# Performance work log

Hardware: AMD Instinct MI355X
Metric: run time of the kernel (lower is better)

Reference implementation:

```python
import jax, jax.numpy as jnp
import numpy as np

N = 16000        # nodes
E = 256000       # edges
D_IN = 1280      # input node features
HID = 256        # hidden dim (all hidden_dims equal; required by res_linear shapes)
HEADS = 8
C = HID // HEADS # 32 channels per head
G = 32           # graphs in the batch
O = 64           # output labels (GO terms)
NB = 2           # conv blocks = len(hidden_dims) - 1
EPS = 1e-5


def _bn(h, g, b):
    # eval-mode BatchNorm1d with running_mean=0, running_var=1 (init state)
    return h * (g / jnp.sqrt(1.0 + EPS)) + b


def _seg_softmax(logits, seg, num):
    # numerically-stable segment softmax (PyG softmax semantics)
    m = jax.ops.segment_max(logits, seg, num_segments=num)
    e = jnp.exp(logits - m[seg])
    s = jax.ops.segment_sum(e, seg, num_segments=num)
    return e / (s[seg] + 1e-16)


def setup_inputs() -> dict:
    key = jax.random.key(0)
    ks = jax.random.split(key, 16)
    w = lambda i, sh: jax.random.normal(ks[i], sh, jnp.float32) * 0.05
    return {
        "x": jax.random.normal(ks[0], (N, D_IN), jnp.float32),
        "edge_index": jax.random.randint(ks[1], (2, E), 0, N),
        "batch": jnp.sort(jax.random.randint(ks[2], (N,), 0, G)),
        # feature_proj: Linear -> ReLU -> BN
        "fp_W": w(3, (D_IN, HID)), "fp_b": jnp.zeros(HID),
        "fp_g": jnp.ones(HID), "fp_be": jnp.zeros(HID),
        # GATv2Conv per block: lin_l, lin_r, att, out-bias
        "gat_Wl": w(4, (NB, HID, HID)), "gat_bl": jnp.zeros((NB, HID)),
        "gat_Wr": w(5, (NB, HID, HID)), "gat_br": jnp.zeros((NB, HID)),
        "gat_att": w(6, (NB, HEADS, C)), "gat_bias": jnp.zeros((NB, HID)),
        # GINConv MLP: Linear -> ReLU -> BN
        "gin_W": w(7, (NB, HID, HID)), "gin_b": jnp.zeros((NB, HID)),
        "gin_g": jnp.ones((NB, HID)), "gin_be": jnp.zeros((NB, HID)),
        # PyG LayerNorm (graph mode) affine
        "ln_g": jnp.ones((NB, HID)), "ln_b": jnp.zeros((NB, HID)),
        # residual linears
        "res_W": w(8, (NB, HID, HID)), "res_b": jnp.zeros((NB, HID)),
        # GlobalAttention gate MLP
        "pool_W1": w(9, (HID, HID)), "pool_b1": jnp.zeros(HID),
        "pool_W2": w(10, (HID, 1)), "pool_b2": jnp.zeros(1),
        # O label heads (hierarchy=None -> just the MLP), stacked
        "head_W1": w(11, (O, HID, 256)), "head_b1": jnp.zeros((O, 256)),
        "head_g": jnp.ones((O, 256)), "head_be": jnp.zeros((O, 256)),
        "head_W2": w(12, (O, 256)), "head_b2": jnp.zeros(O),
    }


def reference(x, edge_index, batch, fp_W, fp_b, fp_g, fp_be,
              gat_Wl, gat_bl, gat_Wr, gat_br, gat_att, gat_bias,
              gin_W, gin_b, gin_g, gin_be, ln_g, ln_b, res_W, res_b,
              pool_W1, pool_b1, pool_W2, pool_b2,
              head_W1, head_b1, head_g, head_be, head_W2, head_b2):
    n = x.shape[0]
    # feature_proj (eval: dropout = identity)
    h = _bn(jax.nn.relu(x @ fp_W + fp_b), fp_g, fp_be)

    src0, dst0 = edge_index[0], edge_index[1]
    loop = jnp.arange(n)
    src = jnp.concatenate([src0, loop])  # GATv2 adds self-loops by default
    dst = jnp.concatenate([dst0, loop])

    for i in range(NB):
        # ---- GATv2Conv (no activation after, per original control flow) ----
        xl = (h @ gat_Wl[i] + gat_bl[i]).reshape(n, HEADS, C)
        xr = (h @ gat_Wr[i] + gat_br[i]).reshape(n, HEADS, C)
        msg = xl[src]                                   # [E', H, C]
        eact = jax.nn.leaky_relu(msg + xr[dst], 0.2)
        logit = jnp.einsum('ehc,hc->eh', eact, gat_att[i])
        alpha = _seg_softmax(logit, dst, n)             # [E', H]
        h = jax.ops.segment_sum(alpha[:, :, None] * msg, dst,
                                num_segments=n).reshape(n, HID) + gat_bias[i]
        # ---- GINConv: nn((1+0)*x + sum_neighbors), then leaky_relu ----
        agg = jax.ops.segment_sum(h[src0], dst0, num_segments=n)
        gin = _bn(jax.nn.relu((h + agg) @ gin_W[i] + gin_b[i]), gin_g[i], gin_be[i])
        h = jax.nn.leaky_relu(gin, 0.2)
        # ---- PyG LayerNorm (graph mode, batch=None: global mean/std) + residual ----
        mu = h.mean()
        sd = jnp.std(h)
        ln = (h - mu) / (sd + EPS) * ln_g[i] + ln_b[i]
        h = jax.nn.leaky_relu(ln + (h @ res_W[i] + res_b[i]), 0.2)

    # ---- GlobalAttention pooling ----
    gate = jnp.tanh(h @ pool_W1 + pool_b1) @ pool_W2 + pool_b2   # [N, 1]
    a = _seg_softmax(gate[:, 0], batch, G)
    emb = jax.ops.segment_sum(a[:, None] * h, batch, num_segments=G)  # [G, HID]

    # ---- O label heads (hierarchy None -> MLP only), vectorized ----
    z = jnp.einsum('bd,odh->boh', emb, head_W1) + head_b1[None]
    z = _bn(jax.nn.silu(z), head_g[None], head_be[None])
    out = jnp.einsum('boh,oh->bo', z, head_W2) + head_b2[None]
    return out[:, :, None]  # torch.stack(outputs, dim=1) -> [G, O, 1]
```

## Files before the change

kernel.cpp:

```cpp
#include <hip/hip_runtime.h>
#include <math.h>

#define N_NODES 16000
#define N_EDGES 256000
#define EPE (N_EDGES + N_NODES)
#define DIN 1280
#define HID 256
#define HEADS 8
#define CPH 32
#define NG 32
#define NO 64
#define EPSC 1e-5f
#define SPAD 40

typedef __bf16 bf16;
typedef __attribute__((ext_vector_type(8))) __bf16 bf16x8;
typedef __attribute__((ext_vector_type(4))) float floatx4;

__device__ __forceinline__ float lrelu(float v) { return v > 0.f ? v : 0.2f * v; }
__device__ __forceinline__ float bflo(unsigned int u) { return __uint_as_float(u << 16); }
__device__ __forceinline__ float bfhi(unsigned int u) { return __uint_as_float(u & 0xffff0000u); }
__device__ __forceinline__ unsigned int bfpack(float x, float y) {
    bf16 b0 = (bf16)x, b1 = (bf16)y;
    return ((unsigned int)*(unsigned short*)&b0) | (((unsigned int)*(unsigned short*)&b1) << 16);
}

__global__ void wconv_gen(const float* __restrict__ W, bf16* __restrict__ Wt, int K, int total) {
    int idx = blockIdx.x * 256 + threadIdx.x;
    if (idx >= total) return;
    int per = K * HID;
    int l = idx / per, rem = idx - l * per;
    int n = rem / K, k = rem - n * K;
    Wt[idx] = (bf16)W[(size_t)l * per + (size_t)k * HID + n];
}

__global__ void wconv_pair(const float* __restrict__ Wl, const float* __restrict__ Wr,
                           bf16* __restrict__ Wt) {
    int idx = blockIdx.x * 256 + threadIdx.x;
    int n = idx >> 8, k = idx & 255;
    float v = (n < 256) ? Wl[(size_t)k * HID + n] : Wr[(size_t)k * HID + (n - 256)];
    Wt[idx] = (bf16)v;
}

__global__ __launch_bounds__(256) void gemm64(
    const bf16* __restrict__ A, const bf16* __restrict__ Bt,
    const float* __restrict__ bias, const float* __restrict__ bias2,
    bf16* __restrict__ C, int K, int ldc, int mode,
    const float* __restrict__ g, const float* __restrict__ be,
    float2* __restrict__ statp, const float* __restrict__ stat)
{
    __shared__ __align__(16) bf16 As[2][64 * SPAD];
    __shared__ __align__(16) bf16 Bs[2][64 * SPAD];
    const int tid = threadIdx.x;
    const int bm = blockIdx.y * 64, bn = blockIdx.x * 64;
    const int w = tid >> 6, lane = tid & 63;
    const int wm = w * 16;
    const int lrow = lane & 15, lk8 = (lane >> 4) * 8;
    const int row = tid >> 2, k8 = (tid & 3) * 8;

    const bf16* gA = A + (size_t)(bm + row) * K + k8;
    const bf16* gB = Bt + (size_t)(bn + row) * K + k8;

    floatx4 acc[4];
#pragma unroll
    for (int j = 0; j < 4; j++) acc[j] = (floatx4){0.f, 0.f, 0.f, 0.f};

    const int nk = K >> 5;
    bf16x8 ra = *(const bf16x8*)gA;
    bf16x8 rb = *(const bf16x8*)gB;

    for (int it = 0; it < nk; ++it) {
        int p = it & 1;
        *(bf16x8*)&As[p][row * SPAD + k8] = ra;
        *(bf16x8*)&Bs[p][row * SPAD + k8] = rb;
        __syncthreads();
        if (it + 1 < nk) {
            ra = *(const bf16x8*)(gA + (it + 1) * 32);
            rb = *(const bf16x8*)(gB + (it + 1) * 32);
        }
        bf16x8 af = *(const bf16x8*)&As[p][(wm + lrow) * SPAD + lk8];
        bf16x8 bfr[4];
#pragma unroll
        for (int j = 0; j < 4; j++) bfr[j] = *(const bf16x8*)&Bs[p][(16 * j + lrow) * SPAD + lk8];
#pragma unroll
        for (int j = 0; j < 4; j++)
            acc[j] = __builtin_amdgcn_mfma_f32_16x16x32_bf16(af, bfr[j], acc[j], 0, 0, 0);
    }

    const float inv = rsqrtf(1.f + EPSC);
    const int row0 = bm + wm + (lane >> 4) * 4;
    float mu = 0.f, rs = 0.f;
    if (mode == 3) {
        const float inv_n = 1.f / (float)((size_t)N_NODES * HID);
        mu = stat[0] * inv_n;
        float var = stat[1] * inv_n - mu * mu;
        rs = 1.f / (sqrtf(fmaxf(var, 0.f)) + EPSC);
    }
    float sz = 0.f, sq = 0.f;
#pragma unroll
    for (int j = 0; j < 4; j++) {
        int col = bn + 16 * j + lrow;
        float bcol = (col < HID) ? bias[col] : bias2[col - HID];
        float gc = (mode >= 2) ? g[col] : 0.f;
        float bec = (mode >= 2) ? be[col] : 0.f;
#pragma unroll
        for (int r = 0; r < 4; r++) {
            float z = acc[j][r] + bcol;
            if (mode == 2) {
                z = fmaxf(z, 0.f) * (gc * inv) + bec;
                z = lrelu(z);
                sz += z; sq += z * z;
            } else if (mode == 3) {
                float h = (float)A[(size_t)(row0 + r) * K + col];
                z = (h - mu) * rs * gc + bec + z;
                z = lrelu(z);
            }
            C[(size_t)(row0 + r) * ldc + col] = (bf16)z;
        }
    }
    if (mode == 2) {
        for (int o = 32; o > 0; o >>= 1) { sz += __shfl_down(sz, o); sq += __shfl_down(sq, o); }
        __syncthreads();
        float* rs_ = (float*)&As[0][0];
        float* rq_ = (float*)&Bs[0][0];
        if (lane == 0) { rs_[w] = sz; rq_[w] = sq; }
        __syncthreads();
        if (tid == 0)
            statp[blockIdx.y * gridDim.x + blockIdx.x] =
                make_float2(rs_[0] + rs_[1] + rs_[2] + rs_[3],
                            rq_[0] + rq_[1] + rq_[2] + rq_[3]);
    }
}

__global__ __launch_bounds__(256, 1) void gemm_f32A(
    const float* __restrict__ A, const bf16* __restrict__ Bt,
    const float* __restrict__ bias, bf16* __restrict__ C, int K,
    const float* __restrict__ g, const float* __restrict__ be)
{
    __shared__ __align__(16) bf16 As[2][128 * SPAD];
    __shared__ __align__(16) bf16 Bs[2][128 * SPAD];
    const int tid = threadIdx.x;
    const int bm = blockIdx.y * 128, bn = blockIdx.x * 128;
    const int w = tid >> 6, lane = tid & 63;
    const int wm = (w & 1) * 64, wn = (w >> 1) * 64;
    const int lrow = lane & 15, lk8 = (lane >> 4) * 8;

    floatx4 acc[4][4];
#pragma unroll
    for (int i = 0; i < 4; i++)
#pragma unroll
        for (int j = 0; j < 4; j++) acc[i][j] = (floatx4){0.f, 0.f, 0.f, 0.f};

    const int r2 = tid >> 1, c2 = tid & 1;
    const float* gA = A + (size_t)(bm + r2) * K + c2 * 16;
    const bf16* gB = Bt + (size_t)(bn + r2) * K + c2 * 16;
    bf16* sA = &As[0][r2 * SPAD + c2 * 16];
    bf16* sB = &Bs[0][r2 * SPAD + c2 * 16];

    const int nk = K >> 5;
    float4 a[4][4];
    bf16x8 b[4][2];
#pragma unroll
    for (int u = 0; u < 4; u++) {
        const float* pa = gA + u * 32;
        a[u][0] = *(const float4*)(pa + 0);
        a[u][1] = *(const float4*)(pa + 4);
        a[u][2] = *(const float4*)(pa + 8);
        a[u][3] = *(const float4*)(pa + 12);
        const bf16* pb = gB + u * 32;
        b[u][0] = *(const bf16x8*)(pb + 0);
        b[u][1] = *(const bf16x8*)(pb + 8);
    }

    for (int it0 = 0; it0 < nk; it0 += 4) {
#pragma unroll
        for (int u = 0; u < 4; u++) {
            const int it = it0 + u;
            const int p = u & 1;
            const int po = p * 128 * SPAD;
            bf16x8 h0, h1;
            h0[0] = (bf16)a[u][0].x; h0[1] = (bf16)a[u][0].y; h0[2] = (bf16)a[u][0].z; h0[3] = (bf16)a[u][0].w;
            h0[4] = (bf16)a[u][1].x; h0[5] = (bf16)a[u][1].y; h0[6] = (bf16)a[u][1].z; h0[7] = (bf16)a[u][1].w;
            h1[0] = (bf16)a[u][2].x; h1[1] = (bf16)a[u][2].y; h1[2] = (bf16)a[u][2].z; h1[3] = (bf16)a[u][2].w;
            h1[4] = (bf16)a[u][3].x; h1[5] = (bf16)a[u][3].y; h1[6] = (bf16)a[u][3].z; h1[7] = (bf16)a[u][3].w;
            *(bf16x8*)(sA + po + 0) = h0;
            *(bf16x8*)(sA + po + 8) = h1;
            *(bf16x8*)(sB + po + 0) = b[u][0];
            *(bf16x8*)(sB + po + 8) = b[u][1];
            __syncthreads();
            if (it + 4 < nk) {
                const float* pa = gA + (it + 4) * 32;
                a[u][0] = *(const float4*)(pa + 0);
                a[u][1] = *(const float4*)(pa + 4);
                a[u][2] = *(const float4*)(pa + 8);
                a[u][3] = *(const float4*)(pa + 12);
                const bf16* pb = gB + (it + 4) * 32;
                b[u][0] = *(const bf16x8*)(pb + 0);
                b[u][1] = *(const bf16x8*)(pb + 8);
            }
            bf16x8 af[4], bfr[4];
#pragma unroll
            for (int i = 0; i < 4; i++) af[i] = *(const bf16x8*)&As[p][(wm + 16 * i + lrow) * SPAD + lk8];
#pragma unroll
            for (int j = 0; j < 4; j++) bfr[j] = *(const bf16x8*)&Bs[p][(wn + 16 * j + lrow) * SPAD + lk8];
#pragma unroll
            for (int i = 0; i < 4; i++)
#pragma unroll
                for (int j = 0; j < 4; j++)
                    acc[i][j] = __builtin_amdgcn_mfma_f32_16x16x32_bf16(af[i], bfr[j], acc[i][j], 0, 0, 0);
        }
    }

    const float inv = rsqrtf(1.f + EPSC);
#pragma unroll
    for (int j = 0; j < 4; j++) {
        int col = bn + wn + 16 * j + lrow;
        float bcol = bias[col];
        float gc = g[col] * inv;
        float bec = be[col];
#pragma unroll
        for (int i = 0; i < 4; i++) {
            int row0 = bm + wm + 16 * i + (lane >> 4) * 4;
#pragma unroll
            for (int r = 0; r < 4; r++) {
                float z = fmaxf(acc[i][j][r] + bcol, 0.f) * gc + bec;
                C[(size_t)(row0 + r) * HID + col] = (bf16)z;
            }
        }
    }
}

__global__ void hist_kernel(const int* __restrict__ ei, int* __restrict__ cnt) {
    int e = blockIdx.x * 256 + threadIdx.x;
    if (e >= EPE) return;
    int d = (e < N_EDGES) ? ei[N_EDGES + e] : (e - N_EDGES);
    atomicAdd(&cnt[d], 1);
}

__global__ __launch_bounds__(1024) void scan_kernel(const int* __restrict__ cnt,
                                                    int* __restrict__ roff, int* __restrict__ cursor,
                                                    const int* __restrict__ batch,
                                                    int* __restrict__ gstart) {
    __shared__ int wsum[16];
    int t = threadIdx.x;
    int base = t * 16;
    int local[16]; int s = 0;
#pragma unroll
    for (int i = 0; i < 16; i++) {
        int idx = base + i;
        int v = (idx < N_NODES) ? cnt[idx] : 0;
        local[i] = s; s += v;
    }
    int lane = t & 63, wid = t >> 6;
    int incl = s;
    for (int o = 1; o < 64; o <<= 1) { int v = __shfl_up(incl, o); if (lane >= o) incl += v; }
    if (lane == 63) wsum[wid] = incl;
    __syncthreads();
    if (t == 0) { int a = 0; for (int k = 0; k < 16; k++) { int v = wsum[k]; wsum[k] = a; a += v; } }
    __syncthreads();
    int texcl = incl - s + wsum[wid];
#pragma unroll
    for (int i = 0; i < 16; i++) {
        int idx = base + i;
        if (idx < N_NODES) { int o = texcl + local[i]; roff[idx] = o; cursor[idx] = o; }
    }
    if (t == 1023) roff[N_NODES] = texcl + s;
    if (t <= NG) {
        int lo = 0, hi = N_NODES;
        while (lo < hi) { int mid = (lo + hi) >> 1; if (batch[mid] < t) lo = mid + 1; else hi = mid; }
        gstart[t] = lo;
    }
}

__global__ void scatter_kernel(const int* __restrict__ ei, int* __restrict__ cursor,
                               int* __restrict__ esrc) {
    int e = blockIdx.x * 256 + threadIdx.x;
    if (e >= EPE) return;
    int s, d;
    if (e < N_EDGES) { s = ei[e]; d = ei[N_EDGES + e]; }
    else { s = d = e - N_EDGES; }
    int pos = atomicAdd(&cursor[d], 1);
    esrc[pos] = s;
}

__global__ __launch_bounds__(256) void gat_wave(
    const bf16* __restrict__ XLR, const int* __restrict__ roff, const int* __restrict__ esrc,
    const float* __restrict__ att, const float* __restrict__ gbias, bf16* __restrict__ out)
{
    const int wid = threadIdx.x >> 6;
    const int lane = threadIdx.x & 63;
    const int d = blockIdx.x * 4 + wid;
    const int beg = roff[d], end = roff[d + 1];
    const int c0 = lane * 4;

    const unsigned int* xru = (const unsigned int*)(XLR + (size_t)d * 512 + 256 + c0);
    const unsigned int xr01 = xru[0], xr23 = xru[1];
    const float xr0 = bflo(xr01), xr1 = bfhi(xr01), xr2 = bflo(xr23), xr3 = bfhi(xr23);
    const float at0 = att[c0], at1 = att[c0 + 1], at2 = att[c0 + 2], at3 = att[c0 + 3];

    float m = -INFINITY, s = 0.f;
    float a0 = 0.f, a1 = 0.f, a2 = 0.f, a3 = 0.f;

    int src = esrc[beg];
    const unsigned int* xp = (const unsigned int*)(XLR + (size_t)src * 512 + c0);
    unsigned int xl01 = xp[0], xl23 = xp[1];

    for (int e = beg; e < end; ++e) {
        unsigned int nx01 = 0u, nx23 = 0u;
        if (e + 1 < end) {
            int ns = esrc[e + 1];
            const unsigned int* np = (const unsigned int*)(XLR + (size_t)ns * 512 + c0);
            nx01 = np[0]; nx23 = np[1];
        }
        float x0 = bflo(xl01), x1 = bfhi(xl01), x2 = bflo(xl23), x3 = bfhi(xl23);
        float p = lrelu(x0 + xr0) * at0 + lrelu(x1 + xr1) * at1
                + lrelu(x2 + xr2) * at2 + lrelu(x3 + xr3) * at3;
        p += __shfl_xor(p, 1);
        p += __shfl_xor(p, 2);
        p += __shfl_xor(p, 4);
        float mn = fmaxf(m, p);
        float rsc = __expf(m - mn);
        float wgt = __expf(p - mn);
        s = s * rsc + wgt;
        a0 = a0 * rsc + wgt * x0;
        a1 = a1 * rsc + wgt * x1;
        a2 = a2 * rsc + wgt * x2;
        a3 = a3 * rsc + wgt * x3;
        m = mn;
        xl01 = nx01; xl23 = nx23;
    }

    const float rinv = 1.f / (s + 1e-16f);
    float v0 = gbias[c0]     + a0 * rinv;
    float v1 = gbias[c0 + 1] + a1 * rinv;
    float v2 = gbias[c0 + 2] + a2 * rinv;
    float v3 = gbias[c0 + 3] + a3 * rinv;
    unsigned int* op = (unsigned int*)(out + (size_t)d * HID + c0);
    op[0] = bfpack(v0, v1);
    op[1] = bfpack(v2, v3);
}

__global__ __launch_bounds__(256) void gin_wave(
    const bf16* __restrict__ H, const int* __restrict__ roff,
    const int* __restrict__ esrc, bf16* __restrict__ U)
{
    const int wid = threadIdx.x >> 6;
    const int lane = threadIdx.x & 63;
    const int d = blockIdx.x * 4 + wid;
    const int beg = roff[d], end = roff[d + 1];
    const int c0 = lane * 4;

    float a0 = 0.f, a1 = 0.f, a2 = 0.f, a3 = 0.f;
    int e = beg;
    for (; e + 1 < end; e += 2) {
        int s0 = esrc[e], s1 = esrc[e + 1];
        const unsigned int* p0 = (const unsigned int*)(H + (size_t)s0 * HID + c0);
        const unsigned int* p1 = (const unsigned int*)(H + (size_t)s1 * HID + c0);
        unsigned int u01 = p0[0], u23 = p0[1];
        unsigned int v01 = p1[0], v23 = p1[1];
        a0 += bflo(u01) + bflo(v01);
        a1 += bfhi(u01) + bfhi(v01);
        a2 += bflo(u23) + bflo(v23);
        a3 += bfhi(u23) + bfhi(v23);
    }
    if (e < end) {
        const unsigned int* p0 = (const unsigned int*)(H + (size_t)esrc[e] * HID + c0);
        unsigned int u01 = p0[0], u23 = p0[1];
        a0 += bflo(u01); a1 += bfhi(u01); a2 += bflo(u23); a3 += bfhi(u23);
    }
    unsigned int* up = (unsigned int*)(U + (size_t)d * HID + c0);
    up[0] = bfpack(a0, a1);
    up[1] = bfpack(a2, a3);
}

__global__ void stats_reduce(const float2* __restrict__ part, float* __restrict__ stat, int n) {
    int t = threadIdx.x;
    float s = 0.f, q = 0.f;
    for (int i = t; i < n; i += 256) { float2 v = part[i]; s += v.x; q += v.y; }
    for (int o = 32; o > 0; o >>= 1) { s += __shfl_down(s, o); q += __shfl_down(q, o); }
    __shared__ float ls[4], lq[4];
    int wid = t >> 6, lane = t & 63;
    if (lane == 0) { ls[wid] = s; lq[wid] = q; }
    __syncthreads();
    if (t == 0) { stat[0] = ls[0] + ls[1] + ls[2] + ls[3]; stat[1] = lq[0] + lq[1] + lq[2] + lq[3]; }
}

__global__ __launch_bounds__(256) void pool_gate_kernel(const bf16* __restrict__ t,
    const float* __restrict__ W2, const float* __restrict__ b2, float* __restrict__ gate)
{
    int n = blockIdx.x * 4 + (threadIdx.x >> 6);
    int lane = threadIdx.x & 63;
    const bf16* p = t + (size_t)n * HID + lane * 4;
    float4 w = *(const float4*)(W2 + lane * 4);
    float s = tanhf((float)p[0]) * w.x + tanhf((float)p[1]) * w.y
            + tanhf((float)p[2]) * w.z + tanhf((float)p[3]) * w.w;
    for (int o = 32; o > 0; o >>= 1) s += __shfl_down(s, o);
    if (lane == 0) gate[n] = s + b2[0];
}

__global__ __launch_bounds__(256) void pool_stats_kernel(
    float* __restrict__ gate, const int* __restrict__ gstart)
{
    int g = blockIdx.x, t = threadIdx.x;
    int lo = gstart[g], hi = gstart[g + 1];
    __shared__ float red[256];
    float m = -INFINITY;
    for (int n = lo + t; n < hi; n += 256) m = fmaxf(m, gate[n]);
    red[t] = m; __syncthreads();
    for (int st = 128; st > 0; st >>= 1) { if (t < st) red[t] = fmaxf(red[t], red[t + st]); __syncthreads(); }
    m = red[0]; __syncthreads();
    float s = 0.f;
    for (int n = lo + t; n < hi; n += 256) s += __expf(gate[n] - m);
    red[t] = s; __syncthreads();
    for (int st = 128; st > 0; st >>= 1) { if (t < st) red[t] += red[t + st]; __syncthreads(); }
    float sinv = 1.f / (red[0] + 1e-16f);
    for (int n = lo + t; n < hi; n += 256) gate[n] = __expf(gate[n] - m) * sinv;
}

__global__ __launch_bounds__(256) void emb_accum_kernel(
    const float* __restrict__ a, const int* __restrict__ batch,
    const bf16* __restrict__ h, float* __restrict__ emb)
{
    int n0 = blockIdx.x * 32, t = threadIdx.x;
    int cur = batch[n0]; float acc = 0.f;
    for (int j = 0; j < 32; j++) {
        int n = n0 + j;
        int b = batch[n];
        if (b != cur) { atomicAdd(&emb[cur * HID + t], acc); cur = b; acc = 0.f; }
        acc += a[n] * (float)h[(size_t)n * HID + t];
    }
    atomicAdd(&emb[cur * HID + t], acc);
}

__global__ __launch_bounds__(256) void heads_kernel(
    const float* __restrict__ emb, const float* __restrict__ W1, const float* __restrict__ b1,
    const float* __restrict__ hg, const float* __restrict__ hbe, const float* __restrict__ W2,
    const float* __restrict__ b2, float* __restrict__ out)
{
    int o = blockIdx.x;
    int g0 = blockIdx.y * 4;
    int k = threadIdx.x;
    __shared__ float se[4][HID];
    __shared__ float red[256];
#pragma unroll
    for (int j = 0; j < 4; j++) se[j][k] = emb[(g0 + j) * HID + k];
    __syncthreads();
    const float* w1p = W1 + (size_t)o * HID * HID + k;
    float zb = b1[o * HID + k];
    float z0 = zb, z1 = zb, z2 = zb, z3 = zb;
#pragma unroll 8
    for (int d = 0; d < HID; d++) {
        float w = w1p[(size_t)d * HID];
        z0 = fmaf(se[0][d], w, z0);
        z1 = fmaf(se[1][d], w, z1);
        z2 = fmaf(se[2][d], w, z2);
        z3 = fmaf(se[3][d], w, z3);
    }
    const float gk = hg[o * HID + k] * rsqrtf(1.f + EPSC);
    const float bek = hbe[o * HID + k];
    const float w2 = W2[o * HID + k];
    const float b2o = b2[o];
    float zz[4] = {z0, z1, z2, z3};
#pragma unroll
    for (int j = 0; j < 4; j++) {
        float z = zz[j];
        float sil = z / (1.f + expf(-z));
        red[k] = (sil * gk + bek) * w2;
        __syncthreads();
        for (int st = 128; st > 0; st >>= 1) { if (k < st) red[k] += red[k + st]; __syncthreads(); }
        if (k == 0) out[(g0 + j) * NO + o] = red[0] + b2o;
        __syncthreads();
    }
}

extern "C" void kernel_launch(void* const* d_in, const int* in_sizes, int n_in,
                              void* d_out, int out_size, void* d_ws, size_t ws_size,
                              hipStream_t stream) {
    const float* x        = (const float*)d_in[0];
    const int*   ei       = (const int*)  d_in[1];
    const int*   batch    = (const int*)  d_in[2];
    const float* fp_W     = (const float*)d_in[3];
    const float* fp_b     = (const float*)d_in[4];
    const float* fp_g     = (const float*)d_in[5];
    const float* fp_be    = (const float*)d_in[6];
    const float* gat_Wl   = (const float*)d_in[7];
    const float* gat_bl   = (const float*)d_in[8];
    const float* gat_Wr   = (const float*)d_in[9];
    const float* gat_br   = (const float*)d_in[10];
    const float* gat_att  = (const float*)d_in[11];
    const float* gat_bias = (const float*)d_in[12];
    const float* gin_W    = (const float*)d_in[13];
    const float* gin_b    = (const float*)d_in[14];
    const float* gin_g    = (const float*)d_in[15];
    const float* gin_be   = (const float*)d_in[16];
    const float* ln_g     = (const float*)d_in[17];
    const float* ln_b     = (const float*)d_in[18];
    const float* res_W    = (const float*)d_in[19];
    const float* res_b    = (const float*)d_in[20];
    const float* pool_W1  = (const float*)d_in[21];
    const float* pool_b1  = (const float*)d_in[22];
    const float* pool_W2  = (const float*)d_in[23];
    const float* pool_b2  = (const float*)d_in[24];
    const float* head_W1  = (const float*)d_in[25];
    const float* head_b1  = (const float*)d_in[26];
    const float* head_g   = (const float*)d_in[27];
    const float* head_be  = (const float*)d_in[28];
    const float* head_W2  = (const float*)d_in[29];
    const float* head_b2  = (const float*)d_in[30];
    float* out = (float*)d_out;

    char* base = (char*)d_ws;
    size_t off = 0;
    auto alloc = [&](size_t bytes) -> char* {
        char* p = base + off; off += (bytes + 255) & ~(size_t)255; return p;
    };
    int*   esrc   = (int*)  alloc((size_t)EPE * 4);
    int*   cnt    = (int*)  alloc((size_t)N_NODES * 4);
    int*   roff   = (int*)  alloc((size_t)(N_NODES + 1) * 4);
    int*   cursor = (int*)  alloc((size_t)N_NODES * 4);
    float* gate   = (float*)alloc((size_t)N_NODES * 4);
    int*   gstart = (int*)  alloc((NG + 1) * 4);
    float* emb    = (float*)alloc(NG * HID * 4);
    float* stat   = (float*)alloc(8);
    float2* statp = (float2*)alloc(1024 * 8);
    bf16*  Hb0    = (bf16*) alloc((size_t)N_NODES * HID * 2);
    bf16*  Hb1    = (bf16*) alloc((size_t)N_NODES * HID * 2);
    bf16*  XLR    = (bf16*) alloc((size_t)N_NODES * 512 * 2);
    bf16*  fpWt   = (bf16*) alloc((size_t)DIN * HID * 2);
    bf16*  wlrT0  = (bf16*) alloc((size_t)512 * HID * 2);
    bf16*  wlrT1  = (bf16*) alloc((size_t)512 * HID * 2);
    bf16*  gwT    = (bf16*) alloc((size_t)2 * HID * HID * 2);
    bf16*  rwT    = (bf16*) alloc((size_t)2 * HID * HID * 2);
    bf16*  pwT    = (bf16*) alloc((size_t)HID * HID * 2);
    bf16*  Ub     = XLR;
    bf16*  wlrT[2] = { wlrT0, wlrT1 };

    wconv_gen<<<(DIN * HID + 255) / 256, 256, 0, stream>>>(fp_W, fpWt, DIN, DIN * HID);
    wconv_pair<<<512, 256, 0, stream>>>(gat_Wl, gat_Wr, wlrT0);
    wconv_pair<<<512, 256, 0, stream>>>(gat_Wl + HID * HID, gat_Wr + HID * HID, wlrT1);
    wconv_gen<<<512, 256, 0, stream>>>(gin_W, gwT, HID, 2 * HID * HID);
    wconv_gen<<<512, 256, 0, stream>>>(res_W, rwT, HID, 2 * HID * HID);
    wconv_gen<<<256, 256, 0, stream>>>(pool_W1, pwT, HID, HID * HID);

    hipMemsetAsync(cnt, 0, N_NODES * sizeof(int), stream);
    hist_kernel<<<(EPE + 255) / 256, 256, 0, stream>>>(ei, cnt);
    scan_kernel<<<1, 1024, 0, stream>>>(cnt, roff, cursor, batch, gstart);
    scatter_kernel<<<(EPE + 255) / 256, 256, 0, stream>>>(ei, cursor, esrc);

    dim3 gridF(2, 125);
    dim3 g64_256(4, 250);
    dim3 g64_512(8, 250);
    gemm_f32A<<<gridF, 256, 0, stream>>>(x, fpWt, fp_b, Hb0, DIN, fp_g, fp_be);

    bf16* hcur = Hb0;
    bf16* hoth = Hb1;
    for (int i = 0; i < 2; i++) {
        gemm64<<<g64_512, 256, 0, stream>>>(hcur, wlrT[i], gat_bl + i * HID, gat_br + i * HID,
                                            XLR, HID, 512, 0, nullptr, nullptr, nullptr, nullptr);
        gat_wave<<<N_NODES / 4, 256, 0, stream>>>(XLR, roff, esrc, gat_att + i * HEADS * CPH,
                                                  gat_bias + i * HID, hoth);
        gin_wave<<<N_NODES / 4, 256, 0, stream>>>(hoth, roff, esrc, Ub);
        gemm64<<<g64_256, 256, 0, stream>>>(Ub, gwT + (size_t)i * HID * HID, gin_b + i * HID,
                                            nullptr, hcur, HID, HID, 2,
                                            gin_g + i * HID, gin_be + i * HID, statp, nullptr);
        stats_reduce<<<1, 256, 0, stream>>>(statp, stat, 1000);
        gemm64<<<g64_256, 256, 0, stream>>>(hcur, rwT + (size_t)i * HID * HID, res_b + i * HID,
                                            nullptr, hoth, HID, HID, 3,
                                            ln_g + i * HID, ln_b + i * HID, nullptr, stat);
        bf16* tmp = hcur; hcur = hoth; hoth = tmp;
    }

    gemm64<<<g64_256, 256, 0, stream>>>(hcur, pwT, pool_b1, nullptr, hoth, HID, HID, 0,
                                        nullptr, nullptr, nullptr, nullptr);
    pool_gate_kernel<<<N_NODES / 4, 256, 0, stream>>>(hoth, pool_W2, pool_b2, gate);
    pool_stats_kernel<<<NG, 256, 0, stream>>>(gate, gstart);
    hipMemsetAsync(emb, 0, NG * HID * sizeof(float), stream);
    emb_accum_kernel<<<N_NODES / 32, 256, 0, stream>>>(gate, batch, hcur, emb);

    dim3 hgrid(NO, 8);
    heads_kernel<<<hgrid, 256, 0, stream>>>(emb, head_W1, head_b1, head_g, head_be,
                                            head_W2, head_b2, out);
}
```

Measured before the change: 562.0 us.

## Merge weight conversions, load full-K tiles in GEMM, use atomic LayerNorm stats

Replaces six weight-transpose launches with one combined kernel. Rewrites the K=256 GEMM to load the whole K extent into shared memory at once, dropping the per-step double-buffer loop and its barriers. The stats_reduce kernel is removed: blocks now atomically add their sums into a global accumulator, which gin_wave zeroes beforehand. This cuts launches and syncs, but adds atomic contention on two floats, makes the float reduction order nondeterministic, and uses more shared memory per block, which may lower occupancy.

```diff
diff --git a/kernel.cpp b/kernel.cpp
--- a/kernel.cpp
+++ b/kernel.cpp
@@ -12,6 +12,7 @@
 #define NO 64
 #define EPSC 1e-5f
 #define SPAD 40
+#define SPK 264
 
 typedef __bf16 bf16;
 typedef __attribute__((ext_vector_type(8))) __bf16 bf16x8;
@@ -25,63 +26,81 @@
     return ((unsigned int)*(unsigned short*)&b0) | (((unsigned int)*(unsigned short*)&b1) << 16);
 }
 
-__global__ void wconv_gen(const float* __restrict__ W, bf16* __restrict__ Wt, int K, int total) {
+__global__ __launch_bounds__(256) void wconv_all(
+    const float* __restrict__ fp_W, const float* __restrict__ gat_Wl,
+    const float* __restrict__ gat_Wr, const float* __restrict__ gin_W,
+    const float* __restrict__ res_W, const float* __restrict__ pool_W1,
+    bf16* __restrict__ fpWt, bf16* __restrict__ wlrT0, bf16* __restrict__ wlrT1,
+    bf16* __restrict__ gwT, bf16* __restrict__ rwT, bf16* __restrict__ pwT)
+{
     int idx = blockIdx.x * 256 + threadIdx.x;
-    if (idx >= total) return;
-    int per = K * HID;
-    int l = idx / per, rem = idx - l * per;
-    int n = rem / K, k = rem - n * K;
-    Wt[idx] = (bf16)W[(size_t)l * per + (size_t)k * HID + n];
-}
-
-__global__ void wconv_pair(const float* __restrict__ Wl, const float* __restrict__ Wr,
-                           bf16* __restrict__ Wt) {
-    int idx = blockIdx.x * 256 + threadIdx.x;
-    int n = idx >> 8, k = idx & 255;
-    float v = (n < 256) ? Wl[(size_t)k * HID + n] : Wr[(size_t)k * HID + (n - 256)];
-    Wt[idx] = (bf16)v;
-}
-
-__global__ __launch_bounds__(256) void gemm64(
+    if (idx < 327680) {
+        int n = idx / 1280, k = idx - n * 1280;
+        fpWt[idx] = (bf16)fp_W[k * 256 + n];
+    } else if (idx < 458752) {
+        int r = idx - 327680; int n = r >> 8, k = r & 255;
+        wlrT0[r] = (bf16)(n < 256 ? gat_Wl[k * 256 + n] : gat_Wr[k * 256 + (n - 256)]);
+    } else if (idx < 589824) {
+        int r = idx - 458752; int n = r >> 8, k = r & 255;
+        wlrT1[r] = (bf16)(n < 256 ? gat_Wl[65536 + k * 256 + n]
+                                  : gat_Wr[65536 + k * 256 + (n - 256)]);
+    } else if (idx < 720896) {
+        int r = idx - 589824; int l = r >> 16, rr = r & 65535;
+        int n = rr >> 8, k = rr & 255;
+        gwT[r] = (bf16)gin_W[l * 65536 + k * 256 + n];
+    } else if (idx < 851968) {
+        int r = idx - 720896; int l = r >> 16, rr = r & 65535;
+        int n = rr >> 8, k = rr & 255;
+        rwT[r] = (bf16)res_W[l * 65536 + k * 256 + n];
+    } else {
+        int r = idx - 851968; int n = r >> 8, k = r & 255;
+        pwT[r] = (bf16)pool_W1[k * 256 + n];
+    }
+}
+
+__global__ __launch_bounds__(256) void gemmk(
     const bf16* __restrict__ A, const bf16* __restrict__ Bt,
     const float* __restrict__ bias, const float* __restrict__ bias2,
-    bf16* __restrict__ C, int K, int ldc, int mode,
+    bf16* __restrict__ C, int ldc, int mode,
     const float* __restrict__ g, const float* __restrict__ be,
-    float2* __restrict__ statp, const float* __restrict__ stat)
-{
-    __shared__ __align__(16) bf16 As[2][64 * SPAD];
-    __shared__ __align__(16) bf16 Bs[2][64 * SPAD];
+    float* __restrict__ stat)
+{
+    __shared__ __align__(16) bf16 As[64 * SPK];
+    __shared__ __align__(16) bf16 Bs[64 * SPK];
     const int tid = threadIdx.x;
     const int bm = blockIdx.y * 64, bn = blockIdx.x * 64;
     const int w = tid >> 6, lane = tid & 63;
     const int wm = w * 16;
     const int lrow = lane & 15, lk8 = (lane >> 4) * 8;
-    const int row = tid >> 2, k8 = (tid & 3) * 8;
-
-    const bf16* gA = A + (size_t)(bm + row) * K + k8;
-    const bf16* gB = Bt + (size_t)(bn + row) * K + k8;
+
+    const int row = tid >> 2;
+    const int kseg = (tid & 3) * 64;
+
+    const bf16* gA = A + (size_t)(bm + row) * HID + kseg;
+    const bf16* gB = Bt + (size_t)(bn + row) * HID + kseg;
+
+    bf16x8 ar[8], br[8];
+#pragma unroll
+    for (int c = 0; c < 8; c++) ar[c] = *(const bf16x8*)(gA + c * 8);
+#pragma unroll
+    for (int c = 0; c < 8; c++) br[c] = *(const bf16x8*)(gB + c * 8);
+#pragma unroll
+    for (int c = 0; c < 8; c++) *(bf16x8*)&As[row * SPK + kseg + c * 8] = ar[c];
+#pragma unroll
+    for (int c = 0; c < 8; c++) *(bf16x8*)&Bs[row * SPK + kseg + c * 8] = br[c];
+    __syncthreads();
 
     floatx4 acc[4];
 #pragma unroll
     for (int j = 0; j < 4; j++) acc[j] = (floatx4){0.f, 0.f, 0.f, 0.f};
 
-    const int nk = K >> 5;
-    bf16x8 ra = *(const bf16x8*)gA;
-    bf16x8 rb = *(const bf16x8*)gB;
-
-    for (int it = 0; it < nk; ++it) {
-        int p = it & 1;
-        *(bf16x8*)&As[p][row * SPAD + k8] = ra;
-        *(bf16x8*)&Bs[p][row * SPAD + k8] = rb;
-        __syncthreads();
-        if (it + 1 < nk) {
-            ra = *(const bf16x8*)(gA + (it + 1) * 32);
-            rb = *(const bf16x8*)(gB + (it + 1) * 32);
-        }
-        bf16x8 af = *(const bf16x8*)&As[p][(wm + lrow) * SPAD + lk8];
+#pragma unroll
+    for (int ks = 0; ks < 8; ks++) {
+        bf16x8 af = *(const bf16x8*)&As[(wm + lrow) * SPK + ks * 32 + lk8];
         bf16x8 bfr[4];
 #pragma unroll
-        for (int j = 0; j < 4; j++) bfr[j] = *(const bf16x8*)&Bs[p][(16 * j + lrow) * SPAD + lk8];
+        for (int j = 0; j < 4; j++)
+            bfr[j] = *(const bf16x8*)&Bs[(16 * j + lrow) * SPK + ks * 32 + lk8];
 #pragma unroll
         for (int j = 0; j < 4; j++)
             acc[j] = __builtin_amdgcn_mfma_f32_16x16x32_bf16(af, bfr[j], acc[j], 0, 0, 0);
@@ -111,7 +130,7 @@
                 z = lrelu(z);
                 sz += z; sq += z * z;
             } else if (mode == 3) {
-                float h = (float)A[(size_t)(row0 + r) * K + col];
+                float h = (float)A[(size_t)(row0 + r) * HID + col];
                 z = (h - mu) * rs * gc + bec + z;
                 z = lrelu(z);
             }
@@ -121,14 +140,14 @@
     if (mode == 2) {
         for (int o = 32; o > 0; o >>= 1) { sz += __shfl_down(sz, o); sq += __shfl_down(sq, o); }
         __syncthreads();
-        float* rs_ = (float*)&As[0][0];
-        float* rq_ = (float*)&Bs[0][0];
+        float* rs_ = (float*)&As[0];
+        float* rq_ = (float*)&Bs[0];
         if (lane == 0) { rs_[w] = sz; rq_[w] = sq; }
         __syncthreads();
-        if (tid == 0)
-            statp[blockIdx.y * gridDim.x + blockIdx.x] =
-                make_float2(rs_[0] + rs_[1] + rs_[2] + rs_[3],
-                            rq_[0] + rq_[1] + rq_[2] + rq_[3]);
+        if (tid == 0) {
+            atomicAdd(&stat[0], rs_[0] + rs_[1] + rs_[2] + rs_[3]);
+            atomicAdd(&stat[1], rq_[0] + rq_[1] + rq_[2] + rq_[3]);
+        }
     }
 }
 
@@ -342,8 +361,9 @@
 
 __global__ __launch_bounds__(256) void gin_wave(
     const bf16* __restrict__ H, const int* __restrict__ roff,
-    const int* __restrict__ esrc, bf16* __restrict__ U)
-{
+    const int* __restrict__ esrc, bf16* __restrict__ U, float* __restrict__ stat)
+{
+    if (blockIdx.x == 0 && threadIdx.x == 0) { stat[0] = 0.f; stat[1] = 0.f; }
     const int wid = threadIdx.x >> 6;
     const int lane = threadIdx.x & 63;
     const int d = blockIdx.x * 4 + wid;
@@ -371,18 +391,6 @@
     unsigned int* up = (unsigned int*)(U + (size_t)d * HID + c0);
     up[0] = bfpack(a0, a1);
     up[1] = bfpack(a2, a3);
-}
-
-__global__ void stats_reduce(const float2* __restrict__ part, float* __restrict__ stat, int n) {
-    int t = threadIdx.x;
-    float s = 0.f, q = 0.f;
-    for (int i = t; i < n; i += 256) { float2 v = part[i]; s += v.x; q += v.y; }
-    for (int o = 32; o > 0; o >>= 1) { s += __shfl_down(s, o); q += __shfl_down(q, o); }
-    __shared__ float ls[4], lq[4];
-    int wid = t >> 6, lane = t & 63;
-    if (lane == 0) { ls[wid] = s; lq[wid] = q; }
-    __syncthreads();
-    if (t == 0) { stat[0] = ls[0] + ls[1] + ls[2] + ls[3]; stat[1] = lq[0] + lq[1] + lq[2] + lq[3]; }
 }
 
 __global__ __launch_bounds__(256) void pool_gate_kernel(const bf16* __restrict__ t,
@@ -522,7 +530,6 @@
     int*   gstart = (int*)  alloc((NG + 1) * 4);
     float* emb    = (float*)alloc(NG * HID * 4);
     float* stat   = (float*)alloc(8);
-    float2* statp = (float2*)alloc(1024 * 8);
     bf16*  Hb0    = (bf16*) alloc((size_t)N_NODES * HID * 2);
     bf16*  Hb1    = (bf16*) alloc((size_t)N_NODES * HID * 2);
     bf16*  XLR    = (bf16*) alloc((size_t)N_NODES * 512 * 2);
@@ -535,12 +542,8 @@
     bf16*  Ub     = XLR;
     bf16*  wlrT[2] = { wlrT0, wlrT1 };
 
-    wconv_gen<<<(DIN * HID + 255) / 256, 256, 0, stream>>>(fp_W, fpWt, DIN, DIN * HID);
-    wconv_pair<<<512, 256, 0, stream>>>(gat_Wl, gat_Wr, wlrT0);
-    wconv_pair<<<512, 256, 0, stream>>>(gat_Wl + HID * HID, gat_Wr + HID * HID, wlrT1);
-    wconv_gen<<<512, 256, 0, stream>>>(gin_W, gwT, HID, 2 * HID * HID);
-    wconv_gen<<<512, 256, 0, stream>>>(res_W, rwT, HID, 2 * HID * HID);
-    wconv_gen<<<256, 256, 0, stream>>>(pool_W1, pwT, HID, HID * HID);
+    wconv_all<<<3584, 256, 0, stream>>>(fp_W, gat_Wl, gat_Wr, gin_W, res_W, pool_W1,
+                                        fpWt, wlrT0, wlrT1, gwT, rwT, pwT);
 
     hipMemsetAsync(cnt, 0, N_NODES * sizeof(int), stream);
     hist_kernel<<<(EPE + 255) / 256, 256, 0, stream>>>(ei, cnt);
@@ -555,23 +558,22 @@
     bf16* hcur = Hb0;
     bf16* hoth = Hb1;
     for (int i = 0; i < 2; i++) {
-        gemm64<<<g64_512, 256, 0, stream>>>(hcur, wlrT[i], gat_bl + i * HID, gat_br + i * HID,
-                                            XLR, HID, 512, 0, nullptr, nullptr, nullptr, nullptr);
+        gemmk<<<g64_512, 256, 0, stream>>>(hcur, wlrT[i], gat_bl + i * HID, gat_br + i * HID,
+                                           XLR, 512, 0, nullptr, nullptr, nullptr);
         gat_wave<<<N_NODES / 4, 256, 0, stream>>>(XLR, roff, esrc, gat_att + i * HEADS * CPH,
                                                   gat_bias + i * HID, hoth);
-        gin_wave<<<N_NODES / 4, 256, 0, stream>>>(hoth, roff, esrc, Ub);
-        gemm64<<<g64_256, 256, 0, stream>>>(Ub, gwT + (size_t)i * HID * HID, gin_b + i * HID,
-                                            nullptr, hcur, HID, HID, 2,
-                                            gin_g + i * HID, gin_be + i * HID, statp, nullptr);
-        stats_reduce<<<1, 256, 0, stream>>>(statp, stat, 1000);
-        gemm64<<<g64_256, 256, 0, stream>>>(hcur, rwT + (size_t)i * HID * HID, res_b + i * HID,
-                                            nullptr, hoth, HID, HID, 3,
-                                            ln_g + i * HID, ln_b + i * HID, nullptr, stat);
+        gin_wave<<<N_NODES / 4, 256, 0, stream>>>(hoth, roff, esrc, Ub, stat);
+        gemmk<<<g64_256, 256, 0, stream>>>(Ub, gwT + (size_t)i * HID * HID, gin_b + i * HID,
+                                           nullptr, hcur, HID, 2,
+                                           gin_g + i * HID, gin_be + i * HID, stat);
+        gemmk<<<g64_256, 256, 0, stream>>>(hcur, rwT + (size_t)i * HID * HID, res_b + i * HID,
+                                           nullptr, hoth, HID, 3,
+                                           ln_g + i * HID, ln_b + i * HID, stat);
         bf16* tmp = hcur; hcur = hoth; hoth = tmp;
     }
 
-    gemm64<<<g64_256, 256, 0, stream>>>(hcur, pwT, pool_b1, nullptr, hoth, HID, HID, 0,
-                                        nullptr, nullptr, nullptr, nullptr);
+    gemmk<<<g64_256, 256, 0, stream>>>(hcur, pwT, pool_b1, nullptr, hoth, HID, 0,
+                                       nullptr, nullptr, nullptr);
     pool_gate_kernel<<<N_NODES / 4, 256, 0, stream>>>(hoth, pool_W2, pool_b2, gate);
     pool_stats_kernel<<<NG, 256, 0, stream>>>(gate, gstart);
     hipMemsetAsync(emb, 0, NG * HID * sizeof(float), stream);
```

New measurement: 625.6 us. 11.3% more time.

## Enlarge bf16 GEMM tiles to 128x128 with 2x2 warp layout and deeper prefetch

Applied to the files above, without the earlier changes.

Replaces the 64x64 GEMM with a 128x128 tile where each of four waves computes a 64x64 sub-tile (4x4 MFMA accumulators), which raises operand reuse from shared memory. Global loads are prefetched four K-steps ahead in registers, and the launch grids and the stats partial count are adjusted to match. The cost is much higher register use and fewer blocks (250 or 500 per GEMM on a 256-CU part), which lowers occupancy and may leave CUs underused.

```diff
diff --git a/kernel.cpp b/kernel.cpp
--- a/kernel.cpp
+++ b/kernel.cpp
@@ -42,53 +42,78 @@
     Wt[idx] = (bf16)v;
 }
 
-__global__ __launch_bounds__(256) void gemm64(
+__global__ __launch_bounds__(256) void gemm128(
     const bf16* __restrict__ A, const bf16* __restrict__ Bt,
     const float* __restrict__ bias, const float* __restrict__ bias2,
     bf16* __restrict__ C, int K, int ldc, int mode,
     const float* __restrict__ g, const float* __restrict__ be,
     float2* __restrict__ statp, const float* __restrict__ stat)
 {
-    __shared__ __align__(16) bf16 As[2][64 * SPAD];
-    __shared__ __align__(16) bf16 Bs[2][64 * SPAD];
+    __shared__ __align__(16) bf16 As[2][128 * SPAD];
+    __shared__ __align__(16) bf16 Bs[2][128 * SPAD];
     const int tid = threadIdx.x;
-    const int bm = blockIdx.y * 64, bn = blockIdx.x * 64;
+    const int bm = blockIdx.y * 128, bn = blockIdx.x * 128;
     const int w = tid >> 6, lane = tid & 63;
-    const int wm = w * 16;
+    const int wm = (w & 1) * 64, wn = (w >> 1) * 64;
     const int lrow = lane & 15, lk8 = (lane >> 4) * 8;
-    const int row = tid >> 2, k8 = (tid & 3) * 8;
-
-    const bf16* gA = A + (size_t)(bm + row) * K + k8;
-    const bf16* gB = Bt + (size_t)(bn + row) * K + k8;
-
-    floatx4 acc[4];
-#pragma unroll
-    for (int j = 0; j < 4; j++) acc[j] = (floatx4){0.f, 0.f, 0.f, 0.f};
+
+    floatx4 acc[4][4];
+#pragma unroll
+    for (int i = 0; i < 4; i++)
+#pragma unroll
+        for (int j = 0; j < 4; j++) acc[i][j] = (floatx4){0.f, 0.f, 0.f, 0.f};
+
+    const int r2 = tid >> 1, c2 = tid & 1;
+    const bf16* gA = A + (size_t)(bm + r2) * K + c2 * 16;
+    const bf16* gB = Bt + (size_t)(bn + r2) * K + c2 * 16;
+    bf16* sA = &As[0][r2 * SPAD + c2 * 16];
+    bf16* sB = &Bs[0][r2 * SPAD + c2 * 16];
 
     const int nk = K >> 5;
-    bf16x8 ra = *(const bf16x8*)gA;
-    bf16x8 rb = *(const bf16x8*)gB;
-
-    for (int it = 0; it < nk; ++it) {
-        int p = it & 1;
-        *(bf16x8*)&As[p][row * SPAD + k8] = ra;
-        *(bf16x8*)&Bs[p][row * SPAD + k8] = rb;
-        __syncthreads();
-        if (it + 1 < nk) {
-            ra = *(const bf16x8*)(gA + (it + 1) * 32);
-            rb = *(const bf16x8*)(gB + (it + 1) * 32);
+    bf16x8 a[4][2], b[4][2];
+#pragma unroll
+    for (int u = 0; u < 4; u++) {
+        const bf16* pa = gA + u * 32;
+        a[u][0] = *(const bf16x8*)(pa + 0);
+        a[u][1] = *(const bf16x8*)(pa + 8);
+        const bf16* pb = gB + u * 32;
+        b[u][0] = *(const bf16x8*)(pb + 0);
+        b[u][1] = *(const bf16x8*)(pb + 8);
+    }
+
+    for (int it0 = 0; it0 < nk; it0 += 4) {
+#pragma unroll
+        for (int u = 0; u < 4; u++) {
+            const int it = it0 + u;
+            const int p = u & 1;
+            const int po = p * 128 * SPAD;
+            *(bf16x8*)(sA + po + 0) = a[u][0];
+            *(bf16x8*)(sA + po + 8) = a[u][1];
+            *(bf16x8*)(sB + po + 0) = b[u][0];
+            *(bf16x8*)(sB + po + 8) = b[u][1];
+            __syncthreads();
+            if (it + 4 < nk) {
+                const bf16* pa = gA + (it + 4) * 32;
+                a[u][0] = *(const bf16x8*)(pa + 0);
+                a[u][1] = *(const bf16x8*)(pa + 8);
+                const bf16* pb = gB + (it + 4) * 32;
+                b[u][0] = *(const bf16x8*)(pb + 0);
+                b[u][1] = *(const bf16x8*)(pb + 8);
+            }
+            bf16x8 af[4], bfr[4];
+#pragma unroll
+            for (int i = 0; i < 4; i++) af[i] = *(const bf16x8*)&As[p][(wm + 16 * i + lrow) * SPAD + lk8];
+#pragma unroll
+            for (int j = 0; j < 4; j++) bfr[j] = *(const bf16x8*)&Bs[p][(wn + 16 * j + lrow) * SPAD + lk8];
+#pragma unroll
+            for (int i = 0; i < 4; i++)
+#pragma unroll
+                for (int j = 0; j < 4; j++)
+                    acc[i][j] = __builtin_amdgcn_mfma_f32_16x16x32_bf16(af[i], bfr[j], acc[i][j], 0, 0, 0);
         }
-        bf16x8 af = *(const bf16x8*)&As[p][(wm + lrow) * SPAD + lk8];
-        bf16x8 bfr[4];
-#pragma unroll
-        for (int j = 0; j < 4; j++) bfr[j] = *(const bf16x8*)&Bs[p][(16 * j + lrow) * SPAD + lk8];
-#pragma unroll
-        for (int j = 0; j < 4; j++)
-            acc[j] = __builtin_amdgcn_mfma_f32_16x16x32_bf16(af, bfr[j], acc[j], 0, 0, 0);
     }
 
     const float inv = rsqrtf(1.f + EPSC);
-    const int row0 = bm + wm + (lane >> 4) * 4;
     float mu = 0.f, rs = 0.f;
     if (mode == 3) {
         const float inv_n = 1.f / (float)((size_t)N_NODES * HID);
@@ -99,23 +124,27 @@
     float sz = 0.f, sq = 0.f;
 #pragma unroll
     for (int j = 0; j < 4; j++) {
-        int col = bn + 16 * j + lrow;
+        int col = bn + wn + 16 * j + lrow;
         float bcol = (col < HID) ? bias[col] : bias2[col - HID];
         float gc = (mode >= 2) ? g[col] : 0.f;
         float bec = (mode >= 2) ? be[col] : 0.f;
 #pragma unroll
-        for (int r = 0; r < 4; r++) {
-            float z = acc[j][r] + bcol;
-            if (mode == 2) {
-                z = fmaxf(z, 0.f) * (gc * inv) + bec;
-                z = lrelu(z);
-                sz += z; sq += z * z;
-            } else if (mode == 3) {
-                float h = (float)A[(size_t)(row0 + r) * K + col];
-                z = (h - mu) * rs * gc + bec + z;
-                z = lrelu(z);
+        for (int i = 0; i < 4; i++) {
+            int row0 = bm + wm + 16 * i + (lane >> 4) * 4;
+#pragma unroll
+            for (int r = 0; r < 4; r++) {
+                float z = acc[i][j][r] + bcol;
+                if (mode == 2) {
+                    z = fmaxf(z, 0.f) * (gc * inv) + bec;
+                    z = lrelu(z);
+                    sz += z; sq += z * z;
+                } else if (mode == 3) {
+                    float h = (float)A[(size_t)(row0 + r) * K + col];
+                    z = (h - mu) * rs * gc + bec + z;
+                    z = lrelu(z);
+                }
+                C[(size_t)(row0 + r) * ldc + col] = (bf16)z;
             }
-            C[(size_t)(row0 + r) * ldc + col] = (bf16)z;
         }
     }
     if (mode == 2) {
@@ -548,30 +577,30 @@
     scatter_kernel<<<(EPE + 255) / 256, 256, 0, stream>>>(ei, cursor, esrc);
 
     dim3 gridF(2, 125);
-    dim3 g64_256(4, 250);
-    dim3 g64_512(8, 250);
+    dim3 g128_256(2, 125);
+    dim3 g128_512(4, 125);
     gemm_f32A<<<gridF, 256, 0, stream>>>(x, fpWt, fp_b, Hb0, DIN, fp_g, fp_be);
 
     bf16* hcur = Hb0;
     bf16* hoth = Hb1;
     for (int i = 0; i < 2; i++) {
-        gemm64<<<g64_512, 256, 0, stream>>>(hcur, wlrT[i], gat_bl + i * HID, gat_br + i * HID,
-                                            XLR, HID, 512, 0, nullptr, nullptr, nullptr, nullptr);
+        gemm128<<<g128_512, 256, 0, stream>>>(hcur, wlrT[i], gat_bl + i * HID, gat_br + i * HID,
+                                              XLR, HID, 512, 0, nullptr, nullptr, nullptr, nullptr);
         gat_wave<<<N_NODES / 4, 256, 0, stream>>>(XLR, roff, esrc, gat_att + i * HEADS * CPH,
                                                   gat_bias + i * HID, hoth);
         gin_wave<<<N_NODES / 4, 256, 0, stream>>>(hoth, roff, esrc, Ub);
-        gemm64<<<g64_256, 256, 0, stream>>>(Ub, gwT + (size_t)i * HID * HID, gin_b + i * HID,
-                                            nullptr, hcur, HID, HID, 2,
-                                            gin_g + i * HID, gin_be + i * HID, statp, nullptr);
-        stats_reduce<<<1, 256, 0, stream>>>(statp, stat, 1000);
-        gemm64<<<g64_256, 256, 0, stream>>>(hcur, rwT + (size_t)i * HID * HID, res_b + i * HID,
-                                            nullptr, hoth, HID, HID, 3,
-                                            ln_g + i * HID, ln_b + i * HID, nullptr, stat);
+        gemm128<<<g128_256, 256, 0, stream>>>(Ub, gwT + (size_t)i * HID * HID, gin_b + i * HID,
+                                              nullptr, hcur, HID, HID, 2,
+                                              gin_g + i * HID, gin_be + i * HID, statp, nullptr);
+        stats_reduce<<<1, 256, 0, stream>>>(statp, stat, 250);
+        gemm128<<<g128_256, 256, 0, stream>>>(hcur, rwT + (size_t)i * HID * HID, res_b + i * HID,
+                                              nullptr, hoth, HID, HID, 3,
+                                              ln_g + i * HID, ln_b + i * HID, nullptr, stat);
         bf16* tmp = hcur; hcur = hoth; hoth = tmp;
     }
 
-    gemm64<<<g64_256, 256, 0, stream>>>(hcur, pwT, pool_b1, nullptr, hoth, HID, HID, 0,
-                                        nullptr, nullptr, nullptr, nullptr);
+    gemm128<<<g128_256, 256, 0, stream>>>(hcur, pwT, pool_b1, nullptr, hoth, HID, HID, 0,
+                                          nullptr, nullptr, nullptr, nullptr);
     pool_gate_kernel<<<N_NODES / 4, 256, 0, stream>>>(hoth, pool_W2, pool_b2, gate);
     pool_stats_kernel<<<NG, 256, 0, stream>>>(gate, gstart);
     hipMemsetAsync(emb, 0, NG * HID * sizeof(float), stream);
```

After: 570.7 us. Within noise of the previous version (+1.6%).
